# Performance work log

Measured on AMD Instinct MI355X. Metric: run time of the kernel, lower is better.

Reference implementation:

```python
import jax, jax.numpy as jnp
import numpy as np

B, T, BIN, D, S, L = 128, 512, 24, 256, 128, 2
MAX_LEN = 512.0   # config.max_length, used as attention score scale
EPS = 1e-6
P = 3.0           # GeM pooling power


def _sinusoid(t, dim, min_ts=1.0, max_ts=10000.0):
    # half sin / half cos geometric timescales (min_timescale..max_timescale)
    num = dim // 2
    inv = min_ts * jnp.exp(jnp.arange(num, dtype=jnp.float32) * (-np.log(max_ts / min_ts) / max(num - 1, 1)))
    ang = jnp.arange(t, dtype=jnp.float32)[:, None] * inv[None, :]        # [T, dim/2]
    return jnp.concatenate([jnp.sin(ang), jnp.cos(ang)], axis=-1)          # [T, dim]


def _rope(x):
    # rotate-half RoPE over last dim, positions along axis -2
    t, d = x.shape[-2], x.shape[-1]
    inv = 1.0 / (10000.0 ** (jnp.arange(0, d, 2, dtype=jnp.float32) / d))  # [d/2]
    ang = jnp.arange(t, dtype=jnp.float32)[:, None] * inv[None, :]         # [T, d/2]
    sin = jnp.concatenate([jnp.sin(ang), jnp.sin(ang)], axis=-1)
    cos = jnp.concatenate([jnp.cos(ang), jnp.cos(ang)], axis=-1)
    x1, x2 = jnp.split(x, 2, axis=-1)
    return x * cos + jnp.concatenate([-x2, x1], axis=-1) * sin


def setup_inputs() -> dict:
    key = jax.random.key(0)
    ks = jax.random.split(key, 12)
    std_in = 1.0 / np.sqrt(BIN)
    std_d = 1.0 / np.sqrt(D)
    return {
        "x": jax.random.uniform(ks[0], (B, T, BIN), dtype=jnp.float32),
        "pe_scale": jnp.ones((), jnp.float32),                                  # learnable PE scale
        "W_in": jax.random.normal(ks[1], (BIN, D), jnp.float32) * std_in,        # encoder_start
        "b_in": jnp.zeros((D,), jnp.float32),
        "norm_scale": jnp.ones((L,), jnp.float32),                               # ScaledNorm scalar per layer
        "W1": jax.random.normal(ks[2], (L, D, 2 * D + S), jnp.float32) * std_d,  # GAU in-proj
        "b1": jnp.zeros((L, 2 * D + S), jnp.float32),
        "gamma": jnp.ones((L, 2, S), jnp.float32),                               # q/k offset-scale
        "beta": jnp.zeros((L, 2, S), jnp.float32),
        "W2": jax.random.normal(ks[3], (L, D, D), jnp.float32) * std_d,          # GAU out-proj
        "b2": jnp.zeros((L, D), jnp.float32),
        "We": jax.random.normal(ks[4], (D, D), jnp.float32) * std_d,             # metric embedding
        "be": jnp.zeros((D,), jnp.float32),
    }


def reference(x, pe_scale, W_in, b_in, norm_scale, W1, b1, gamma, beta, W2, b2, We, be):
    # scaled sinusoidal positional embedding (additive)
    h = x + pe_scale * _sinusoid(x.shape[1], x.shape[2])
    # encoder start + swish
    h = jax.nn.swish(h @ W_in + b_in)                                   # [B,T,D]
    for i in range(L):  # GAU stack (attention-free gated attention units)
        shortcut = h
        hn = h * jax.lax.rsqrt(jnp.mean(h * h, axis=-1, keepdims=True) + EPS) * norm_scale[i]
        uv = jax.nn.swish(hn @ W1[i] + b1[i])                           # [B,T,2D+S]
        u, v, base = uv[..., :D], uv[..., D:2 * D], uv[..., 2 * D:]
        q = _rope(base * gamma[i, 0] + beta[i, 0])                      # [B,T,S]
        k = _rope(base * gamma[i, 1] + beta[i, 1])
        scores = jnp.einsum('bnd,bmd->bnm', q, k) / MAX_LEN             # [B,T,T]
        attn = jnp.square(jax.nn.relu(scores))                          # SqrReLU
        out = u * jnp.einsum('bnm,bme->bne', attn, v)                   # gated attention output
        h = shortcut + out @ W2[i] + b2[i]
    unpooled = h
    # generalized-mean pooling over sequence (p=3, clamp for stability)
    pooled = jnp.mean(jnp.clip(h, EPS, None) ** P, axis=1) ** (1.0 / P)  # [B,D]
    # metric embedding: linear + L2 normalize
    emb = pooled @ We + be
    emb = emb / jnp.linalg.norm(emb, axis=-1, keepdims=True)
    return emb, unpooled
```

## Files before the change

### kernel.cpp

```cpp
#include <hip/hip_runtime.h>
#include <hip/hip_bf16.h>

#define B_ 128
#define T_ 512
#define BIN_ 24
#define D_ 256
#define S_ 128
#define L_ 2
#define BT_ (B_*T_)

typedef __hip_bfloat16 bf16;
typedef __hip_bfloat162 bf162;
typedef __attribute__((ext_vector_type(8))) short bf16x8;
typedef __attribute__((ext_vector_type(4))) short s16x4;
typedef __attribute__((ext_vector_type(4))) float f32x4;

__device__ __forceinline__ float b2f(bf16 x){ return __bfloat162float(x); }
__device__ __forceinline__ bf16 f2b(float x){ return __float2bfloat16(x); }
__device__ __forceinline__ float swish(float v){
  float e = __builtin_amdgcn_exp2f(-1.442695040888963f * v);
  return v * __builtin_amdgcn_rcpf(1.f + e);
}
__device__ __forceinline__ void gld16(const bf16* g, bf16* l){
  __builtin_amdgcn_global_load_lds(
      (const __attribute__((address_space(1))) void*)g,
      (__attribute__((address_space(3))) void*)l, 16, 0, 0);
}

__global__ void tables_kernel(const float* pe_scale_ptr, float* pe_tab, float* rs, float* rc) {
  int t = blockIdx.x;
  int j = threadIdx.x;
  float ps = pe_scale_ptr[0];
  const float LOG1E4 = 9.210340371976184f;
  if (j < 64) {
    float inv = expf(-LOG1E4 * (float)j / 64.f);
    float ang = (float)t * inv;
    rs[t*64 + j] = sinf(ang);
    rc[t*64 + j] = cosf(ang);
  }
  if (j < BIN_) {
    int jj = (j < 12) ? j : (j - 12);
    float inv = expf(-LOG1E4 * (float)jj / 11.f);
    float ang = (float)t * inv;
    pe_tab[t*BIN_ + j] = ps * ((j < 12) ? sinf(ang) : cosf(ang));
  }
}

__global__ __launch_bounds__(256) void prep_kernel(const float* W1, const float* W2,
                                                   bf16* W1t, bf16* W2t) {
  int idx = blockIdx.x*256 + threadIdx.x;
  if (idx < 2*256*640) {
    int l = idx / (256*640); int rem = idx % (256*640);
    int k = rem / 640; int n = rem % 640;
    W1t[(size_t)l*640*256 + n*256 + k] = f2b(W1[idx]);
  }
  if (idx < 2*256*256) {
    int l = idx >> 16; int rem = idx & 65535;
    int k = rem >> 8; int n = rem & 255;
    W2t[(size_t)l*65536 + n*256 + k] = f2b(W2[idx]);
  }
}

__global__ __launch_bounds__(256) void init_kernel(float* rms1, float* pooled_raw) {
  int i = blockIdx.x*256 + threadIdx.x;
  if (i < BT_) rms1[i] = 0.f;
  if (i < B_*D_) pooled_raw[i] = 0.f;
}

__global__ __launch_bounds__(256) void embed_kernel(const float* x, const float* pe_tab,
                const float* W_in, const float* b_in, float* h, float* rms0, bf16* hb) {
  __shared__ float xr[8][BIN_];
  __shared__ float wsum[4][8];
  int tid = threadIdx.x;
  int row0 = blockIdx.x * 8;
  if (tid < 8*BIN_) {
    int r = tid / BIN_, k = tid % BIN_;
    int row = row0 + r;
    int t = row & (T_-1);
    xr[r][k] = x[(size_t)row*BIN_ + k] + pe_tab[t*BIN_ + k];
  }
  __syncthreads();
  int d = tid;
  float bi = b_in[d];
  float acc[8];
  #pragma unroll
  for (int r=0;r<8;r++) acc[r]=bi;
  #pragma unroll
  for (int k=0;k<BIN_;k++){
    float w = W_in[k*D_ + d];
    #pragma unroll
    for (int r=0;r<8;r++) acc[r] += xr[r][k]*w;
  }
  float sq[8];
  #pragma unroll
  for (int r=0;r<8;r++){
    float v = swish(acc[r]);
    h[(size_t)(row0+r)*D_ + d] = v;
    hb[(size_t)(row0+r)*D_ + d] = f2b(v);
    sq[r] = v*v;
  }
  #pragma unroll
  for (int off=1; off<64; off<<=1)
    #pragma unroll
    for (int r=0;r<8;r++) sq[r] += __shfl_xor(sq[r], off);
  if ((tid&63)==0)
    #pragma unroll
    for (int r=0;r<8;r++) wsum[tid>>6][r] = sq[r];
  __syncthreads();
  if (tid < 8) rms0[row0+tid] = wsum[0][tid]+wsum[1][tid]+wsum[2][tid]+wsum[3][tid];
}

__global__ __launch_bounds__(256) void gemm1_mfma(const bf16* A, const bf16* Bt,
      const float* bias, const float* rmsraw, const float* norm_scale, int l,
      bf16* u, bf16* Vtg, bf16* basebuf) {
  __shared__ char smem[34816];
  bf16* As  = (bf16*)smem;
  bf16* Bs  = (bf16*)(smem + 16384);
  bf16* Ovl = (bf16*)smem;

  int tid = threadIdx.x;
  int w = tid>>6, lane = tid&63, r = lane&15, g = lane>>4;
  int wr = w>>1, wc = w&1;
  int dd = blockIdx.x; int xcd = dd&7, slot = dd>>3;
  int panel = xcd*64 + slot/5; int bx = slot%5;
  int row0 = panel*128, col0 = bx*128;

  int trl = 8*w + (lane>>3);
  int tcg = ((lane&7) ^ ((lane>>3)&7)) * 8;

  f32x4 acc[4][4];
  #pragma unroll
  for (int i=0;i<4;i++)
    #pragma unroll
    for (int j=0;j<4;j++) acc[i][j] = (f32x4){0.f,0.f,0.f,0.f};

  for (int k0=0; k0<D_; k0+=64) {
    #pragma unroll
    for (int i=0;i<4;i++){
      int tr = 32*i + trl;
      gld16(A  + (size_t)(row0+tr)*D_ + k0 + tcg, As + (32*i + 8*w)*64);
      gld16(Bt + (size_t)(col0+tr)*D_ + k0 + tcg, Bs + (32*i + 8*w)*64);
    }
    __syncthreads();
    #pragma unroll
    for (int kk=0; kk<2; kk++){
      bf16x8 a[4], b[4];
      #pragma unroll
      for (int i=0;i<4;i++){
        int ch = ((kk*4 + g) ^ (r&7)) * 8;
        a[i] = *(const bf16x8*)(As + (64*wr+16*i+r)*64 + ch);
        b[i] = *(const bf16x8*)(Bs + (64*wc+16*i+r)*64 + ch);
      }
      #pragma unroll
      for (int i=0;i<4;i++)
        #pragma unroll
        for (int j=0;j<4;j++)
          acc[i][j] = __builtin_amdgcn_mfma_f32_16x16x32_bf16(a[i], b[j], acc[i][j], 0,0,0);
    }
    __syncthreads();
  }

  float ns = norm_scale[l];
  #pragma unroll
  for (int i=0;i<4;i++){
    size_t grow0 = row0 + 64*wr + 16*i + 4*g;
    float4 rv = *(const float4*)(rmsraw + grow0);
    float sc[4];
    sc[0] = rsqrtf(rv.x*(1.f/D_) + 1e-6f) * ns;
    sc[1] = rsqrtf(rv.y*(1.f/D_) + 1e-6f) * ns;
    sc[2] = rsqrtf(rv.z*(1.f/D_) + 1e-6f) * ns;
    sc[3] = rsqrtf(rv.w*(1.f/D_) + 1e-6f) * ns;
    #pragma unroll
    for (int j=0;j<4;j++){
      int gcol = col0 + 64*wc + 16*j + r;
      float bv = bias[gcol];
      if (bx < 2) {
        #pragma unroll
        for (int reg=0; reg<4; reg++){
          float v = swish(acc[i][j][reg]*sc[reg] + bv);
          u[(grow0+reg)*D_ + gcol] = f2b(v);
        }
      } else if (bx < 4) {
        #pragma unroll
        for (int reg=0; reg<4; reg++){
          float v = swish(acc[i][j][reg]*sc[reg] + bv);
          Ovl[(64*wc+16*j+r)*136 + (64*wr+16*i+4*g+reg)] = f2b(v);
        }
      } else {
        #pragma unroll
        for (int reg=0; reg<4; reg++){
          float v = swish(acc[i][j][reg]*sc[reg] + bv);
          basebuf[(grow0+reg)*S_ + (gcol-512)] = f2b(v);
        }
      }
    }
  }

  if (bx == 2 || bx == 3) {
    __syncthreads();
    size_t bb = row0 >> 9;
    int mg = row0 & 511;
    #pragma unroll
    for (int c=0;c<8;c++){
      int chunk = c*256 + tid;
      int e = chunk >> 4, mloc = (chunk & 15)*8;
      *(bf16x8*)(Vtg + bb*131072 + (size_t)(col0-256+e)*T_ + mg + mloc) =
        *(const bf16x8*)(Ovl + e*136 + mloc);
    }
  }
}

__global__ __launch_bounds__(256) void qk_kernel(const bf16* basebuf, const float* gamma, const float* beta,
      int l, const float* rs, const float* rc, bf16* q, bf16* k) {
  int tid = threadIdx.x;
  int j = tid & 127;
  size_t row = (size_t)blockIdx.x*2 + (tid>>7);
  int t = (int)(row & (T_-1));
  int j2 = j ^ 64;
  float v0 = b2f(basebuf[row*S_ + j]);
  float v1 = b2f(basebuf[row*S_ + j2]);
  int jm = j & 63;
  float sn = rs[t*64 + jm], cs = rc[t*64 + jm];
  float sgn = (j < 64) ? -1.f : 1.f;
  const float* g  = gamma + l*2*S_;
  const float* bt = beta  + l*2*S_;
  float xq = v0*g[j]      + bt[j];
  float pq = v1*g[j2]     + bt[j2];
  q[row*S_ + j] = f2b(xq*cs + sgn*pq*sn);
  float xk = v0*g[S_+j]   + bt[S_+j];
  float pk = v1*g[S_+j2]  + bt[S_+j2];
  k[row*S_ + j] = f2b(xk*cs + sgn*pk*sn);
}

__global__ __launch_bounds__(512, 4) void attn_gemm2_fused(const bf16* q, const bf16* k,
      const bf16* Vtg, const bf16* u, const bf16* W2t, const float* bias,
      float* h, int mode, float* rms1, float* pooled_raw, float* outb, bf16* hb) {
  __shared__ char smem[77824];
  bf16* Ks = (bf16*)smem;
  bf16* Vt = (bf16*)(smem + 16384);
  bf16* Ps = (bf16*)(smem + 49152);
  bf16* Os = (bf16*)smem;
  bf16* Wt = (bf16*)(smem + 67584);

  int tid = threadIdx.x;
  int w = tid >> 6, l = tid & 63;
  int r = l & 15, g = l >> 4;
  int xcd = blockIdx.x & 7, j0 = blockIdx.x >> 3;
  int b  = xcd*16 + (j0 >> 2);
  int nt = j0 & 3;
  size_t rowbase = (size_t)b * T_;
  int n0 = nt * 128;

  bf16x8 qf[4];
  const bf16* qrow = q + (rowbase + n0 + 16*w + r) * S_ + g*8;
  #pragma unroll
  for (int kk=0; kk<4; kk++) qf[kk] = *(const bf16x8*)(qrow + kk*32);

  f32x4 oacc[16];
  #pragma unroll
  for (int i=0;i<16;i++) oacc[i] = (f32x4){0.f,0.f,0.f,0.f};

  for (int m0 = 0; m0 < T_; m0 += 64) {
    #pragma unroll
    for (int i=0;i<2;i++){
      int chunk = i*512 + w*64 + l;
      int row = chunk >> 4, c = chunk & 15;
      gld16(k + (rowbase + m0 + row)*S_ + ((c ^ (row&7)) << 3),
            Ks + (i*512 + w*64)*8);
    }
    #pragma unroll
    for (int i=0;i<4;i++){
      int chunk = i*512 + w*64 + l;
      int e = chunk >> 3, c = chunk & 7;
      gld16(Vtg + (size_t)b*131072 + (size_t)e*T_ + m0 + ((c ^ (e&7)) << 3),
            Vt + (i*512 + w*64)*8);
    }
    __syncthreads();

    #pragma unroll
    for (int nf=0; nf<4; nf++){
      f32x4 sacc = (f32x4){0.f,0.f,0.f,0.f};
      #pragma unroll
      for (int kk=0; kk<4; kk++){
        int ch = ((kk*4 + g) ^ (r&7)) * 8;
        bf16x8 kf = *(const bf16x8*)(Ks + (16*nf + r)*128 + ch);
        sacc = __builtin_amdgcn_mfma_f32_16x16x32_bf16(qf[kk], kf, sacc, 0,0,0);
      }
      #pragma unroll
      for (int reg=0; reg<4; reg++){
        float t = fmaxf(sacc[reg] * (1.f/512.f), 0.f);
        Ps[(16*w + 4*g + reg)*72 + 16*nf + r] = f2b(t*t);
      }
    }
    #pragma unroll
    for (int ks=0; ks<2; ks++){
      bf16x8 pa = *(const bf16x8*)(Ps + (16*w + r)*72 + ks*32 + g*8);
      #pragma unroll
      for (int nf2=0; nf2<16; nf2++){
        int e = 16*nf2 + r;
        bf16x8 vb = *(const bf16x8*)(Vt + e*64 + (((4*ks + g) ^ (e&7)) << 3));
        oacc[nf2] = __builtin_amdgcn_mfma_f32_16x16x32_bf16(pa, vb, oacc[nf2], 0,0,0);
      }
    }
    __syncthreads();
  }

  size_t growbase = rowbase + n0;
  #pragma unroll
  for (int nf2=0; nf2<16; nf2++){
    #pragma unroll
    for (int reg=0; reg<4; reg++){
      Os[(16*w + 4*g + reg)*264 + 16*nf2 + r] = f2b(oacc[nf2][reg]);
    }
  }
  __syncthreads();
  #pragma unroll
  for (int i=0;i<8;i++){
    int chunk = i*512 + tid;
    int row = chunk >> 5, c = chunk & 31;
    bf16x8 uvv = *(const bf16x8*)(u + (growbase + row)*D_ + c*8);
    bf16x8 ov  = *(const bf16x8*)(Os + row*264 + c*8);
    bf16x8 res;
    #pragma unroll
    for (int e=0;e<8;e++)
      ((bf16*)&res)[e] = f2b(b2f(((bf16*)&ov)[e]) * b2f(((bf16*)&uvv)[e]));
    *(bf16x8*)(Os + row*264 + c*8) = res;
  }
  #pragma unroll
  for (int i=0;i<16;i++) oacc[i] = (f32x4){0.f,0.f,0.f,0.f};
  __syncthreads();

  for (int kc=0; kc<8; kc++){
    bf16x8 a0 = *(const bf16x8*)(Os + (16*w + r)*264 + kc*32 + g*8);
    #pragma unroll
    for (int nh=0; nh<2; nh++){
      __syncthreads();
      {
        int rowW = tid>>2, ko = (tid&3)*8;
        *(bf16x8*)(Wt + rowW*40 + ko) =
          *(const bf16x8*)(W2t + (size_t)(128*nh + rowW)*256 + kc*32 + ko);
      }
      __syncthreads();
      #pragma unroll
      for (int nf2h=0; nf2h<8; nf2h++){
        bf16x8 bfr = *(const bf16x8*)(Wt + (16*nf2h + r)*40 + g*8);
        oacc[nh*8+nf2h] =
          __builtin_amdgcn_mfma_f32_16x16x32_bf16(a0, bfr, oacc[nh*8+nf2h], 0,0,0);
      }
    }
  }

  if (mode == 0) {
    #pragma unroll
    for (int reg=0; reg<4; reg++){
      size_t row = growbase + 16*w + 4*g + reg;
      float ssum = 0.f;
      #pragma unroll
      for (int nf2=0; nf2<16; nf2++){
        int col = 16*nf2 + r;
        float hv = h[row*D_ + col] + oacc[nf2][reg] + bias[col];
        h[row*D_ + col] = hv;
        hb[row*D_ + col] = f2b(hv);
        ssum += hv*hv;
      }
      ssum += __shfl_xor(ssum,1); ssum += __shfl_xor(ssum,2);
      ssum += __shfl_xor(ssum,4); ssum += __shfl_xor(ssum,8);
      if (r == 0) rms1[row] = ssum;
    }
  } else {
    #pragma unroll
    for (int nf2=0; nf2<16; nf2++){
      int col = 16*nf2 + r;
      float bv = bias[col];
      float psum = 0.f;
      #pragma unroll
      for (int reg=0; reg<4; reg++){
        size_t row = growbase + 16*w + 4*g + reg;
        float hv = h[row*D_ + col] + oacc[nf2][reg] + bv;
        outb[row*D_ + col] = hv;
        float cv = fmaxf(hv, 1e-6f);
        psum += cv*cv*cv;
      }
      psum += __shfl_xor(psum,16); psum += __shfl_xor(psum,32);
      if (g == 0) atomicAdd(pooled_raw + b*D_ + col, psum);
    }
  }
}

__global__ __launch_bounds__(256) void emb_kernel(const float* pooled_raw, const float* We,
      const float* be, float* out) {
  __shared__ float pr[D_];
  __shared__ float red[256];
  int b = blockIdx.x, j = threadIdx.x;
  pr[j] = cbrtf(pooled_raw[b*D_+j] * (1.f/T_));
  __syncthreads();
  float acc = be[j];
  for (int kk=0;kk<D_;kk++) acc += pr[kk]*We[kk*D_+j];
  red[j] = acc*acc;
  __syncthreads();
  for (int off=128; off>0; off>>=1){
    if (j<off) red[j]+=red[j+off];
    __syncthreads();
  }
  out[b*D_+j] = acc * rsqrtf(red[0]);
}

extern "C" void kernel_launch(void* const* d_in, const int* in_sizes, int n_in,
                              void* d_out, int out_size, void* d_ws, size_t ws_size,
                              hipStream_t stream) {
  const float* x         = (const float*)d_in[0];
  const float* pe_scale  = (const float*)d_in[1];
  const float* W_in      = (const float*)d_in[2];
  const float* b_in      = (const float*)d_in[3];
  const float* norm_scale= (const float*)d_in[4];
  const float* W1        = (const float*)d_in[5];
  const float* b1        = (const float*)d_in[6];
  const float* gamma     = (const float*)d_in[7];
  const float* beta      = (const float*)d_in[8];
  const float* W2        = (const float*)d_in[9];
  const float* b2        = (const float*)d_in[10];
  const float* We        = (const float*)d_in[11];
  const float* be        = (const float*)d_in[12];

  char* ws = (char*)d_ws;
  float* h       = (float*)(ws);
  bf16*  hb      = (bf16*)(ws + 67108864);
  bf16*  u       = (bf16*)(ws + 100663296);
  bf16*  Vtg     = (bf16*)(ws + 134217728);
  bf16*  basebuf = (bf16*)(ws + 167772160);
  bf16*  q       = (bf16*)(ws + 184549376);
  bf16*  kbuf    = (bf16*)(ws + 201326592);
  float* pe_tab  = (float*)(ws + 218103808);
  float* rs_tab  = (float*)(ws + 218152960);
  float* rc_tab  = (float*)(ws + 218284032);
  float* pooled_raw = (float*)(ws + 218415104);
  float* rms0    = (float*)(ws + 218546176);
  float* rms1    = (float*)(ws + 218808320);
  bf16*  W1t     = (bf16*)(ws + 219070464);
  bf16*  W2t     = (bf16*)(ws + 219725824);

  tables_kernel<<<T_, 64, 0, stream>>>(pe_scale, pe_tab, rs_tab, rc_tab);
  prep_kernel<<<1280, 256, 0, stream>>>(W1, W2, W1t, W2t);
  init_kernel<<<BT_/256, 256, 0, stream>>>(rms1, pooled_raw);
  embed_kernel<<<BT_/8, 256, 0, stream>>>(x, pe_tab, W_in, b_in, h, rms0, hb);
  float* outb = (float*)d_out + B_*D_;
  for (int l=0; l<L_; l++) {
    gemm1_mfma<<<BT_/128*5, 256, 0, stream>>>(hb, W1t + (size_t)l*640*D_, b1 + l*640,
        l ? rms1 : rms0, norm_scale, l, u, Vtg, basebuf);
    qk_kernel<<<BT_/2, 256, 0, stream>>>(basebuf, gamma, beta, l, rs_tab, rc_tab, q, kbuf);
    attn_gemm2_fused<<<B_*4, 512, 0, stream>>>(q, kbuf, Vtg, u,
        W2t + (size_t)l*D_*D_, b2 + l*D_, h, l, rms1, pooled_raw, outb, hb);
  }
  emb_kernel<<<B_, 256, 0, stream>>>(pooled_raw, We, be, (float*)d_out);
}
```

Baseline: 354.2 us.

## Repartition out-projection GEMM by columns with W2 fragments held in registers

The out-projection GEMM inside the fused attention kernel changes its split. Each wave now owns 16 output columns across all 128 rows, instead of 16 rows across all columns. The wave loads its W2 fragments straight from global memory into registers and reads the gated activations from LDS. This drops the LDS staging buffer for W2 and the 16 block-wide barriers around it, and shrinks the shared allocation. In exchange, the row sum-of-squares for the next layer's norm is now built with many global atomicAdds per row instead of one store, which depends on rms1 being zeroed beforehand.

```diff
diff --git a/kernel.cpp b/kernel.cpp
--- a/kernel.cpp
+++ b/kernel.cpp
@@ -235,12 +235,11 @@
 __global__ __launch_bounds__(512, 4) void attn_gemm2_fused(const bf16* q, const bf16* k,
       const bf16* Vtg, const bf16* u, const bf16* W2t, const float* bias,
       float* h, int mode, float* rms1, float* pooled_raw, float* outb, bf16* hb) {
-  __shared__ char smem[77824];
+  __shared__ char smem[67584];
   bf16* Ks = (bf16*)smem;
   bf16* Vt = (bf16*)(smem + 16384);
   bf16* Ps = (bf16*)(smem + 49152);
   bf16* Os = (bf16*)smem;
-  bf16* Wt = (bf16*)(smem + 67584);
 
   int tid = threadIdx.x;
   int w = tid >> 6, l = tid & 63;
@@ -326,60 +325,55 @@
       ((bf16*)&res)[e] = f2b(b2f(((bf16*)&ov)[e]) * b2f(((bf16*)&uvv)[e]));
     *(bf16x8*)(Os + row*264 + c*8) = res;
   }
-  #pragma unroll
-  for (int i=0;i<16;i++) oacc[i] = (f32x4){0.f,0.f,0.f,0.f};
-  __syncthreads();
-
-  for (int kc=0; kc<8; kc++){
-    bf16x8 a0 = *(const bf16x8*)(Os + (16*w + r)*264 + kc*32 + g*8);
-    #pragma unroll
-    for (int nh=0; nh<2; nh++){
-      __syncthreads();
-      {
-        int rowW = tid>>2, ko = (tid&3)*8;
-        *(bf16x8*)(Wt + rowW*40 + ko) =
-          *(const bf16x8*)(W2t + (size_t)(128*nh + rowW)*256 + kc*32 + ko);
-      }
-      __syncthreads();
-      #pragma unroll
-      for (int nf2h=0; nf2h<8; nf2h++){
-        bf16x8 bfr = *(const bf16x8*)(Wt + (16*nf2h + r)*40 + g*8);
-        oacc[nh*8+nf2h] =
-          __builtin_amdgcn_mfma_f32_16x16x32_bf16(a0, bfr, oacc[nh*8+nf2h], 0,0,0);
-      }
-    }
-  }
-
-  if (mode == 0) {
-    #pragma unroll
-    for (int reg=0; reg<4; reg++){
-      size_t row = growbase + 16*w + 4*g + reg;
-      float ssum = 0.f;
-      #pragma unroll
-      for (int nf2=0; nf2<16; nf2++){
-        int col = 16*nf2 + r;
-        float hv = h[row*D_ + col] + oacc[nf2][reg] + bias[col];
-        h[row*D_ + col] = hv;
-        hb[row*D_ + col] = f2b(hv);
-        ssum += hv*hv;
-      }
-      ssum += __shfl_xor(ssum,1); ssum += __shfl_xor(ssum,2);
-      ssum += __shfl_xor(ssum,4); ssum += __shfl_xor(ssum,8);
-      if (r == 0) rms1[row] = ssum;
-    }
-  } else {
-    #pragma unroll
-    for (int nf2=0; nf2<16; nf2++){
-      int col = 16*nf2 + r;
-      float bv = bias[col];
+  __syncthreads();
+
+  #pragma unroll
+  for (int chf=0; chf<2; chf++){
+    int col = 128*chf + 16*w + r;
+    bf16x8 wfr[8];
+    #pragma unroll
+    for (int kc=0; kc<8; kc++)
+      wfr[kc] = *(const bf16x8*)(W2t + (size_t)col*256 + kc*32 + g*8);
+    f32x4 acc2[8];
+    #pragma unroll
+    for (int i=0;i<8;i++) acc2[i] = (f32x4){0.f,0.f,0.f,0.f};
+    #pragma unroll
+    for (int kc=0; kc<8; kc++){
+      #pragma unroll
+      for (int i=0;i<8;i++){
+        bf16x8 a0 = *(const bf16x8*)(Os + (16*i + r)*264 + kc*32 + g*8);
+        acc2[i] = __builtin_amdgcn_mfma_f32_16x16x32_bf16(a0, wfr[kc], acc2[i], 0,0,0);
+      }
+    }
+
+    float bv = bias[col];
+    if (mode == 0) {
+      #pragma unroll
+      for (int i=0;i<8;i++){
+        #pragma unroll
+        for (int reg=0; reg<4; reg++){
+          size_t row = growbase + 16*i + 4*g + reg;
+          float hv = h[row*D_ + col] + acc2[i][reg] + bv;
+          h[row*D_ + col] = hv;
+          hb[row*D_ + col] = f2b(hv);
+          float ssum = hv*hv;
+          ssum += __shfl_xor(ssum,1); ssum += __shfl_xor(ssum,2);
+          ssum += __shfl_xor(ssum,4); ssum += __shfl_xor(ssum,8);
+          if (r == 0) atomicAdd(rms1 + row, ssum);
+        }
+      }
+    } else {
       float psum = 0.f;
       #pragma unroll
-      for (int reg=0; reg<4; reg++){
-        size_t row = growbase + 16*w + 4*g + reg;
-        float hv = h[row*D_ + col] + oacc[nf2][reg] + bv;
-        outb[row*D_ + col] = hv;
-        float cv = fmaxf(hv, 1e-6f);
-        psum += cv*cv*cv;
+      for (int i=0;i<8;i++){
+        #pragma unroll
+        for (int reg=0; reg<4; reg++){
+          size_t row = growbase + 16*i + 4*g + reg;
+          float hv = h[row*D_ + col] + acc2[i][reg] + bv;
+          outb[row*D_ + col] = hv;
+          float cv = fmaxf(hv, 1e-6f);
+          psum += cv*cv*cv;
+        }
       }
       psum += __shfl_xor(psum,16); psum += __shfl_xor(psum,32);
       if (g == 0) atomicAdd(pooled_raw + b*D_ + col, psum);
```

New measurement: 348.4 us. No clear change (-1.6%).
